# Kernel optimization log

Hardware: AMD Instinct MI355X
Metric: run time of the kernel (lower is better)

The kernel has to match this reference:

```python
import jax, jax.numpy as jnp
import numpy as np

EPS_F = 1e-6   # epsilon_F global in original repo
GAMMA = 0.8
K = 5
BN_EPS = 1e-5
M = 128
N = 100000
E = 1600000
MY = 10

def setup_inputs() -> dict:
    key = jax.random.key(0)
    ks = jax.random.split(key, 6)
    X = jax.random.normal(ks[0], (M, N), dtype=jnp.float32)
    # xavier_uniform for F: limit = sqrt(6/(m+m))
    lim = float(np.sqrt(6.0 / (M + M)))
    F_mat = jax.random.uniform(ks[1], (M, M), dtype=jnp.float32, minval=-lim, maxval=lim)
    B = (1.0 / np.sqrt(M)) * jax.random.normal(ks[2], (MY, M), dtype=jnp.float32)
    bn_weight = jnp.ones((M,), dtype=jnp.float32)
    bn_bias = jnp.zeros((M,), dtype=jnp.float32)
    edge_val = jax.random.uniform(ks[3], (E,), dtype=jnp.float32)
    edge_row = jax.random.randint(ks[4], (E,), 0, N, dtype=jnp.int64 if jax.config.jax_enable_x64 else jnp.int32)
    edge_col = jax.random.randint(ks[5], (E,), 0, N, dtype=jnp.int64 if jax.config.jax_enable_x64 else jnp.int32)
    return {"X": X, "F_mat": F_mat, "B": B, "bn_weight": bn_weight,
            "bn_bias": bn_bias, "edge_val": edge_val,
            "edge_row": edge_row, "edge_col": edge_col}

def reference(X, F_mat, B, bn_weight, bn_bias, edge_val, edge_row, edge_col):
    n = X.shape[1]
    # normalized Gram matrix g(F) = F^T F / (||F^T F||_fro + eps)
    FF = F_mat.T @ F_mat                       # [m, m]
    G = FF / (jnp.linalg.norm(FF) + EPS_F)
    X_first = X                                # [m, n]

    def step(Xc, _):
        Y = Xc.T                               # [n, m]
        # SpMM: (S_t @ Y)[r] += val * Y[c]
        SY = jax.ops.segment_sum(edge_val[:, None] * Y[edge_col], edge_row,
                                 num_segments=n)   # [n, m]
        Xn = GAMMA * (G @ SY.T) + X_first          # [m, n]
        return Xn, None

    Xk, _ = jax.lax.scan(step, X, None, length=K)
    out = Xk.T                                 # [n, m]
    # BatchNorm1d over feature dim (training-mode batch stats); dropout omitted (eval)
    mu = out.mean(axis=0)
    var = out.var(axis=0)
    out = (out - mu) * jax.lax.rsqrt(var + BN_EPS) * bn_weight + bn_bias
    return out @ B.T                           # [n, m_y]
```

## Files before the change

### kernel.cpp

```cpp
#include <hip/hip_runtime.h>
#include <math.h>

#define MDIM 128
#define MY 10
#define GAMMA 0.8f
#define KITER 5
#define CSHIFT 13
#define CCHUNK 13
#define SCAN_BLK 8192

__device__ __forceinline__ float bf2f(unsigned short h) {
    return __uint_as_float(((unsigned int)h) << 16);
}
__device__ __forceinline__ unsigned short f2bf(float f) {
    unsigned int u = __float_as_uint(f);
    u += 0x7fffu + ((u >> 16) & 1u);
    return (unsigned short)(u >> 16);
}

__global__ void k_transpose(const float* __restrict__ X, float* __restrict__ Y0,
                            unsigned short* __restrict__ Y0h, int n) {
    __shared__ float tile[32][33];
    int r0 = blockIdx.x * 32;
    int f0 = blockIdx.y * 32;
    int tx = threadIdx.x, ty = threadIdx.y;
    #pragma unroll
    for (int i = 0; i < 32; i += 8) {
        tile[ty + i][tx] = X[(size_t)(f0 + ty + i) * n + (r0 + tx)];
    }
    __syncthreads();
    #pragma unroll
    for (int i = 0; i < 32; i += 8) {
        float v = tile[tx][ty + i];
        Y0[(size_t)(r0 + ty + i) * MDIM + (f0 + tx)] = v;
        Y0h[(size_t)(r0 + ty + i) * MDIM + (f0 + tx)] = f2bf(v);
    }
}

__global__ void k_gram(const float* __restrict__ F, float* __restrict__ FF,
                       float* __restrict__ normAcc) {
    int i = blockIdx.x, j = threadIdx.x;
    float acc = 0.f;
    for (int k = 0; k < MDIM; ++k)
        acc = fmaf(F[k * MDIM + i], F[k * MDIM + j], acc);
    FF[i * MDIM + j] = acc;
    __shared__ float red[MDIM];
    red[j] = acc * acc;
    __syncthreads();
    for (int s = 64; s > 0; s >>= 1) {
        if (j < s) red[j] += red[j + s];
        __syncthreads();
    }
    if (j == 0) atomicAdd(normAcc, red[0]);
}

__global__ void k_gnorm(const float* __restrict__ FF, const float* __restrict__ normAcc,
                        float* __restrict__ G) {
    int idx = blockIdx.x * 256 + threadIdx.x;
    float s = GAMMA / (sqrtf(*normAcc) + 1e-6f);
    G[idx] = FF[idx] * s;
}

__global__ void k_hist(const int* __restrict__ erow, const int* __restrict__ ecol,
                       int* __restrict__ cnt, int E) {
    int e = blockIdx.x * 256 + threadIdx.x;
    if (e < E) atomicAdd(&cnt[erow[e] * CCHUNK + (ecol[e] >> CSHIFT)], 1);
}

__global__ void k_scan1(const int* __restrict__ cnt, int* __restrict__ blockSums, int nC) {
    int tid = threadIdx.x;
    int base = blockIdx.x * SCAN_BLK + tid * 32;
    int s = 0;
    if (base + 31 < nC) {
        #pragma unroll
        for (int i = 0; i < 8; ++i) {
            int4 v = *(const int4*)&cnt[base + i * 4];
            s += v.x + v.y + v.z + v.w;
        }
    } else {
        for (int i = 0; i < 32; ++i)
            if (base + i < nC) s += cnt[base + i];
    }
    __shared__ int red[256];
    red[tid] = s;
    __syncthreads();
    for (int st = 128; st > 0; st >>= 1) {
        if (tid < st) red[tid] += red[tid + st];
        __syncthreads();
    }
    if (tid == 0) blockSums[blockIdx.x] = red[0];
}

__global__ void k_scan2(int* __restrict__ blockSums, int* __restrict__ rc_off,
                        int nb, int nC) {
    __shared__ int s[256];
    int tid = threadIdx.x;
    int v = (tid < nb) ? blockSums[tid] : 0;
    s[tid] = v;
    __syncthreads();
    for (int off = 1; off < 256; off <<= 1) {
        int t = (tid >= off) ? s[tid - off] : 0;
        __syncthreads();
        s[tid] += t;
        __syncthreads();
    }
    if (tid < nb) blockSums[tid] = s[tid] - v;
    if (tid == 0) rc_off[nC] = s[255];
}

__global__ void k_scan3(const int* __restrict__ cnt, const int* __restrict__ blockOff,
                        int* __restrict__ rc_off, int nC) {
    int tid = threadIdx.x;
    int base = blockIdx.x * SCAN_BLK + tid * 32;
    int v[32];
    #pragma unroll
    for (int i = 0; i < 32; ++i) v[i] = (base + i < nC) ? cnt[base + i] : 0;
    int local = 0;
    #pragma unroll
    for (int i = 0; i < 32; ++i) local += v[i];
    __shared__ int s[256];
    s[tid] = local;
    __syncthreads();
    for (int off = 1; off < 256; off <<= 1) {
        int t = (tid >= off) ? s[tid - off] : 0;
        __syncthreads();
        s[tid] += t;
        __syncthreads();
    }
    int excl = s[tid] - local + blockOff[blockIdx.x];
    #pragma unroll
    for (int i = 0; i < 32; ++i) {
        if (base + i < nC) { rc_off[base + i] = excl; excl += v[i]; }
    }
}

__global__ void k_scatter(const int* __restrict__ erow, const int* __restrict__ ecol,
                          const float* __restrict__ eval_, int* __restrict__ cursor,
                          int2* __restrict__ csr_cv, int E) {
    int e = blockIdx.x * 256 + threadIdx.x;
    if (e < E) {
        int r = erow[e];
        int c = ecol[e];
        int pos = atomicAdd(&cursor[r * CCHUNK + (c >> CSHIFT)], 1);
        csr_cv[pos] = make_int2(c << 8, __float_as_int(eval_[e]));
    }
}

__global__ void __launch_bounds__(256, 8) k_fused(const unsigned short* __restrict__ Yh,
                                                  const int* __restrict__ rc_off,
                                                  const int2* __restrict__ csr_cv,
                                                  const float* __restrict__ G,
                                                  const float* __restrict__ Y0,
                                                  float* __restrict__ Yout,
                                                  unsigned short* __restrict__ Yhout,
                                                  float* __restrict__ stats,
                                                  int writeH, int writeF, int n) {
    __shared__ float sSY[32 * MDIM];
    int tid = threadIdx.x;
    int ty = tid >> 5;
    int tx = tid & 31;
    int rbase = blockIdx.x * 32;
    const char* yb = (const char*)Yh;
    int lbo = tx * 8;

    for (int i = 0; i < 4; ++i) {
        int rloc = ty * 4 + i;
        int e0 = rc_off[(rbase + rloc) * CCHUNK];
        int e1 = rc_off[(rbase + rloc) * CCHUNK + CCHUNK];
        float4 a = make_float4(0.f, 0.f, 0.f, 0.f);
        int e = e0;
        for (; e + 4 <= e1; e += 4) {
            int2 p0 = csr_cv[e + 0];
            int2 p1 = csr_cv[e + 1];
            int2 p2 = csr_cv[e + 2];
            int2 p3 = csr_cv[e + 3];
            ushort4 h0 = *(const ushort4*)(yb + (size_t)(p0.x + lbo));
            ushort4 h1 = *(const ushort4*)(yb + (size_t)(p1.x + lbo));
            ushort4 h2 = *(const ushort4*)(yb + (size_t)(p2.x + lbo));
            ushort4 h3 = *(const ushort4*)(yb + (size_t)(p3.x + lbo));
            float v0 = __int_as_float(p0.y);
            float v1 = __int_as_float(p1.y);
            float v2 = __int_as_float(p2.y);
            float v3 = __int_as_float(p3.y);
            a.x = fmaf(v0, bf2f(h0.x), a.x);
            a.y = fmaf(v0, bf2f(h0.y), a.y);
            a.z = fmaf(v0, bf2f(h0.z), a.z);
            a.w = fmaf(v0, bf2f(h0.w), a.w);
            a.x = fmaf(v1, bf2f(h1.x), a.x);
            a.y = fmaf(v1, bf2f(h1.y), a.y);
            a.z = fmaf(v1, bf2f(h1.z), a.z);
            a.w = fmaf(v1, bf2f(h1.w), a.w);
            a.x = fmaf(v2, bf2f(h2.x), a.x);
            a.y = fmaf(v2, bf2f(h2.y), a.y);
            a.z = fmaf(v2, bf2f(h2.z), a.z);
            a.w = fmaf(v2, bf2f(h2.w), a.w);
            a.x = fmaf(v3, bf2f(h3.x), a.x);
            a.y = fmaf(v3, bf2f(h3.y), a.y);
            a.z = fmaf(v3, bf2f(h3.z), a.z);
            a.w = fmaf(v3, bf2f(h3.w), a.w);
        }
        for (; e < e1; ++e) {
            int2 p = csr_cv[e];
            float v = __int_as_float(p.y);
            ushort4 h = *(const ushort4*)(yb + (size_t)(p.x + lbo));
            a.x = fmaf(v, bf2f(h.x), a.x);
            a.y = fmaf(v, bf2f(h.y), a.y);
            a.z = fmaf(v, bf2f(h.z), a.z);
            a.w = fmaf(v, bf2f(h.w), a.w);
        }
        *(float4*)&sSY[rloc * MDIM + tx * 4] = a;
    }

    size_t r0 = (size_t)rbase + ty * 4;
    int f0 = tx * 4;
    float4 acc[4];
    #pragma unroll
    for (int i = 0; i < 4; ++i) acc[i] = make_float4(0.f, 0.f, 0.f, 0.f);

    for (int j = 0; j < MDIM; j += 4) {
        float4 g0 = *(const float4*)&G[(j + 0) * MDIM + f0];
        float4 g1 = *(const float4*)&G[(j + 1) * MDIM + f0];
        float4 g2 = *(const float4*)&G[(j + 2) * MDIM + f0];
        float4 g3 = *(const float4*)&G[(j + 3) * MDIM + f0];
        #pragma unroll
        for (int i = 0; i < 4; ++i) {
            float4 sr = *(const float4*)&sSY[(ty * 4 + i) * MDIM + j];
            acc[i].x = fmaf(sr.x, g0.x, acc[i].x);
            acc[i].y = fmaf(sr.x, g0.y, acc[i].y);
            acc[i].z = fmaf(sr.x, g0.z, acc[i].z);
            acc[i].w = fmaf(sr.x, g0.w, acc[i].w);
            acc[i].x = fmaf(sr.y, g1.x, acc[i].x);
            acc[i].y = fmaf(sr.y, g1.y, acc[i].y);
            acc[i].z = fmaf(sr.y, g1.z, acc[i].z);
            acc[i].w = fmaf(sr.y, g1.w, acc[i].w);
            acc[i].x = fmaf(sr.z, g2.x, acc[i].x);
            acc[i].y = fmaf(sr.z, g2.y, acc[i].y);
            acc[i].z = fmaf(sr.z, g2.z, acc[i].z);
            acc[i].w = fmaf(sr.z, g2.w, acc[i].w);
            acc[i].x = fmaf(sr.w, g3.x, acc[i].x);
            acc[i].y = fmaf(sr.w, g3.y, acc[i].y);
            acc[i].z = fmaf(sr.w, g3.z, acc[i].z);
            acc[i].w = fmaf(sr.w, g3.w, acc[i].w);
        }
    }

    float4 bs = make_float4(0.f, 0.f, 0.f, 0.f);
    float4 bq = make_float4(0.f, 0.f, 0.f, 0.f);
    #pragma unroll
    for (int i = 0; i < 4; ++i) {
        float4 y0 = *(const float4*)&Y0[(r0 + i) * MDIM + f0];
        float4 o;
        o.x = acc[i].x + y0.x;
        o.y = acc[i].y + y0.y;
        o.z = acc[i].z + y0.z;
        o.w = acc[i].w + y0.w;
        if (writeF) {
            *(float4*)&Yout[(r0 + i) * MDIM + f0] = o;
            bs.x += o.x; bs.y += o.y; bs.z += o.z; bs.w += o.w;
            bq.x = fmaf(o.x, o.x, bq.x);
            bq.y = fmaf(o.y, o.y, bq.y);
            bq.z = fmaf(o.z, o.z, bq.z);
            bq.w = fmaf(o.w, o.w, bq.w);
        }
        if (writeH) {
            ushort4 h;
            h.x = f2bf(o.x);
            h.y = f2bf(o.y);
            h.z = f2bf(o.z);
            h.w = f2bf(o.w);
            *(ushort4*)&Yhout[(r0 + i) * MDIM + f0] = h;
        }
    }

    if (writeF) {
        __syncthreads();
        *(float4*)&sSY[ty * MDIM + f0] = bs;
        *(float4*)&sSY[8 * MDIM + ty * MDIM + f0] = bq;
        __syncthreads();
        if (tid < MDIM) {
            float a = 0.f, b = 0.f;
            #pragma unroll
            for (int t = 0; t < 8; ++t) {
                a += sSY[t * MDIM + tid];
                b += sSY[8 * MDIM + t * MDIM + tid];
            }
            atomicAdd(&stats[tid], a);
            atomicAdd(&stats[MDIM + tid], b);
        }
    }
}

__global__ void k_finalize(const float* __restrict__ stats, const float* __restrict__ B,
                           const float* __restrict__ bnw, const float* __restrict__ bnb,
                           float* __restrict__ Bs, float* __restrict__ cvec, int n) {
    int f = threadIdx.x;
    float inv_n = 1.f / (float)n;
    float mu = stats[f] * inv_n;
    float var = stats[MDIM + f] * inv_n - mu * mu;
    float rs = rsqrtf(var + 1e-5f);
    float sw = rs * bnw[f];
    float cv = bnb[f] - mu * sw;
    __shared__ float red[MDIM];
    for (int o = 0; o < MY; ++o) {
        float b = B[o * MDIM + f];
        Bs[o * MDIM + f] = b * sw;
        red[f] = b * cv;
        __syncthreads();
        for (int s = 64; s > 0; s >>= 1) {
            if (f < s) red[f] += red[f + s];
            __syncthreads();
        }
        if (f == 0) cvec[o] = red[0];
        __syncthreads();
    }
}

__global__ void __launch_bounds__(256) k_project(const float* __restrict__ Y,
                                                 const float* __restrict__ Bs,
                                                 const float* __restrict__ cvec,
                                                 float* __restrict__ out, int n) {
    __shared__ float yt[16 * 129];
    __shared__ float sB[MY * 129];
    __shared__ float sc[MY];
    int tid = threadIdx.x;
    size_t rbase = (size_t)blockIdx.x * 16;
    for (int idx = tid; idx < 16 * MDIM; idx += 256) {
        int r = idx >> 7, f = idx & 127;
        yt[r * 129 + f] = Y[(rbase + r) * MDIM + f];
    }
    for (int idx = tid; idx < MY * MDIM; idx += 256) {
        int o = idx >> 7, f = idx & 127;
        sB[o * 129 + f] = Bs[idx];
    }
    if (tid < MY) sc[tid] = cvec[tid];
    __syncthreads();
    if (tid < 16 * MY) {
        int r = tid / MY, o = tid % MY;
        float acc = sc[o];
        for (int f = 0; f < MDIM; ++f)
            acc = fmaf(yt[r * 129 + f], sB[o * 129 + f], acc);
        out[(rbase + r) * MY + o] = acc;
    }
}

extern "C" void kernel_launch(void* const* d_in, const int* in_sizes, int n_in,
                              void* d_out, int out_size, void* d_ws, size_t ws_size,
                              hipStream_t stream) {
    const float* X    = (const float*)d_in[0];
    const float* F    = (const float*)d_in[1];
    const float* B    = (const float*)d_in[2];
    const float* bnw  = (const float*)d_in[3];
    const float* bnb  = (const float*)d_in[4];
    const float* ev   = (const float*)d_in[5];
    const int*   erow = (const int*)d_in[6];
    const int*   ecol = (const int*)d_in[7];
    float* out = (float*)d_out;
    const int n = in_sizes[0] / MDIM;
    const int E = in_sizes[5];
    const int nC = n * CCHUNK;

    char* w = (char*)d_ws;
    size_t off = 0;
    auto carve = [&](size_t bytes) -> void* {
        void* p = w + off;
        off += (bytes + 255) & ~(size_t)255;
        return p;
    };
    float*          Y0    = (float*)carve((size_t)n * MDIM * 4);
    float*          Ycur  = (float*)carve((size_t)n * MDIM * 4);
    unsigned short* Yh_a  = (unsigned short*)carve((size_t)n * MDIM * 2);
    unsigned short* Yh_b  = (unsigned short*)carve((size_t)n * MDIM * 2);
    float* FF        = (float*)carve(MDIM * MDIM * 4);
    float* G         = (float*)carve(MDIM * MDIM * 4);
    int2*  csr_cv    = (int2*)carve((size_t)E * 8);
    int*   rc_off    = (int*)carve((size_t)(nC + 1) * 4);
    int*   cursor    = (int*)carve((size_t)nC * 4);
    int*   cnt       = (int*)carve((size_t)nC * 4);
    int*   blockSums = (int*)carve(1024 * 4);
    float* normAcc   = (float*)carve(4);
    float* stats     = (float*)carve(2 * MDIM * 4);
    float* Bs        = (float*)carve(MY * MDIM * 4);
    float* cvec      = (float*)carve(MY * 4);
    (void)ws_size;

    hipMemsetAsync(cnt, 0, (size_t)nC * 4, stream);
    hipMemsetAsync(normAcc, 0, 4, stream);
    hipMemsetAsync(stats, 0, 2 * MDIM * 4, stream);

    k_transpose<<<dim3(n / 32, MDIM / 32), dim3(32, 8), 0, stream>>>(X, Y0, Yh_a, n);
    k_gram<<<MDIM, MDIM, 0, stream>>>(F, FF, normAcc);
    k_gnorm<<<MDIM * MDIM / 256, 256, 0, stream>>>(FF, normAcc, G);

    const int nb = (nC + SCAN_BLK - 1) / SCAN_BLK;
    k_hist<<<(E + 255) / 256, 256, 0, stream>>>(erow, ecol, cnt, E);
    k_scan1<<<nb, 256, 0, stream>>>(cnt, blockSums, nC);
    k_scan2<<<1, 256, 0, stream>>>(blockSums, rc_off, nb, nC);
    k_scan3<<<nb, 256, 0, stream>>>(cnt, blockSums, rc_off, nC);
    hipMemcpyAsync(cursor, rc_off, (size_t)nC * 4, hipMemcpyDeviceToDevice, stream);
    k_scatter<<<(E + 255) / 256, 256, 0, stream>>>(erow, ecol, ev, cursor, csr_cv, E);

    for (int k = 0; k < KITER; ++k) {
        const unsigned short* hin = (k & 1) ? Yh_b : Yh_a;
        unsigned short*       hout = (k & 1) ? Yh_a : Yh_b;
        int writeH = (k < KITER - 1) ? 1 : 0;
        int writeF = (k == KITER - 1) ? 1 : 0;
        k_fused<<<n / 32, 256, 0, stream>>>(hin, rc_off, csr_cv, G, Y0, Ycur, hout,
                                            stats, writeH, writeF, n);
    }

    k_finalize<<<1, MDIM, 0, stream>>>(stats, B, bnw, bnb, Bs, cvec, n);
    k_project<<<n / 16, 256, 0, stream>>>(Ycur, Bs, cvec, out, n);
}
```

Before: 934.0 us.

## Reorder CSR chunk-major, process 64 rows per block with interleaved edge streams

The CSR bucketing changes from row-major to column-chunk-major, so each chunk's edges across all rows are grouped and the gathered Y columns stay within an 8K-row window that can remain in cache. Each block now handles two 32-row tiles and walks four rows' edge lists at once, giving more independent gathers in flight. Intermediate iterations read the X_first residual as bf16 instead of fp32 to cut traffic. This costs more rc_off lookups, loop overhead from the chunk loop and per-edge branches, and adds bf16 rounding to the residual in the early iterations.

```diff
diff --git a/kernel.cpp b/kernel.cpp
--- a/kernel.cpp
+++ b/kernel.cpp
@@ -19,7 +19,8 @@
 }
 
 __global__ void k_transpose(const float* __restrict__ X, float* __restrict__ Y0,
-                            unsigned short* __restrict__ Y0h, int n) {
+                            unsigned short* __restrict__ Y0h,
+                            unsigned short* __restrict__ Yh0, int n) {
     __shared__ float tile[32][33];
     int r0 = blockIdx.x * 32;
     int f0 = blockIdx.y * 32;
@@ -32,8 +33,10 @@
     #pragma unroll
     for (int i = 0; i < 32; i += 8) {
         float v = tile[tx][ty + i];
+        unsigned short h = f2bf(v);
         Y0[(size_t)(r0 + ty + i) * MDIM + (f0 + tx)] = v;
-        Y0h[(size_t)(r0 + ty + i) * MDIM + (f0 + tx)] = f2bf(v);
+        Y0h[(size_t)(r0 + ty + i) * MDIM + (f0 + tx)] = h;
+        Yh0[(size_t)(r0 + ty + i) * MDIM + (f0 + tx)] = h;
     }
 }
 
@@ -62,9 +65,9 @@
 }
 
 __global__ void k_hist(const int* __restrict__ erow, const int* __restrict__ ecol,
-                       int* __restrict__ cnt, int E) {
+                       int* __restrict__ cnt, int E, int n) {
     int e = blockIdx.x * 256 + threadIdx.x;
-    if (e < E) atomicAdd(&cnt[erow[e] * CCHUNK + (ecol[e] >> CSHIFT)], 1);
+    if (e < E) atomicAdd(&cnt[(ecol[e] >> CSHIFT) * n + erow[e]], 1);
 }
 
 __global__ void k_scan1(const int* __restrict__ cnt, int* __restrict__ blockSums, int nC) {
@@ -136,21 +139,33 @@
 
 __global__ void k_scatter(const int* __restrict__ erow, const int* __restrict__ ecol,
                           const float* __restrict__ eval_, int* __restrict__ cursor,
-                          int2* __restrict__ csr_cv, int E) {
+                          int2* __restrict__ csr_cv, int E, int n) {
     int e = blockIdx.x * 256 + threadIdx.x;
     if (e < E) {
         int r = erow[e];
         int c = ecol[e];
-        int pos = atomicAdd(&cursor[r * CCHUNK + (c >> CSHIFT)], 1);
+        int pos = atomicAdd(&cursor[(c >> CSHIFT) * n + r], 1);
         csr_cv[pos] = make_int2(c << 8, __float_as_int(eval_[e]));
     }
 }
+
+#define EDGE_STEP(eCur, eEnd, acc)                                        \
+    if (eCur < eEnd) {                                                    \
+        int2 p = csr_cv[eCur++];                                          \
+        float v = __int_as_float(p.y);                                    \
+        ushort4 h = *(const ushort4*)(yb + (size_t)(p.x + lbo));          \
+        acc.x = fmaf(v, bf2f(h.x), acc.x);                                \
+        acc.y = fmaf(v, bf2f(h.y), acc.y);                                \
+        acc.z = fmaf(v, bf2f(h.z), acc.z);                                \
+        acc.w = fmaf(v, bf2f(h.w), acc.w);                                \
+    }
 
 __global__ void __launch_bounds__(256, 8) k_fused(const unsigned short* __restrict__ Yh,
                                                   const int* __restrict__ rc_off,
                                                   const int2* __restrict__ csr_cv,
                                                   const float* __restrict__ G,
                                                   const float* __restrict__ Y0,
+                                                  const unsigned short* __restrict__ Y0h,
                                                   float* __restrict__ Yout,
                                                   unsigned short* __restrict__ Yhout,
                                                   float* __restrict__ stats,
@@ -159,116 +174,118 @@
     int tid = threadIdx.x;
     int ty = tid >> 5;
     int tx = tid & 31;
-    int rbase = blockIdx.x * 32;
+    int rbase0 = blockIdx.x * 64;
+    int rbase1 = rbase0 + 32;
+    bool hasT1 = (rbase1 < n);
     const char* yb = (const char*)Yh;
     int lbo = tx * 8;
 
-    for (int i = 0; i < 4; ++i) {
-        int rloc = ty * 4 + i;
-        int e0 = rc_off[(rbase + rloc) * CCHUNK];
-        int e1 = rc_off[(rbase + rloc) * CCHUNK + CCHUNK];
-        float4 a = make_float4(0.f, 0.f, 0.f, 0.f);
-        int e = e0;
-        for (; e + 4 <= e1; e += 4) {
-            int2 p0 = csr_cv[e + 0];
-            int2 p1 = csr_cv[e + 1];
-            int2 p2 = csr_cv[e + 2];
-            int2 p3 = csr_cv[e + 3];
-            ushort4 h0 = *(const ushort4*)(yb + (size_t)(p0.x + lbo));
-            ushort4 h1 = *(const ushort4*)(yb + (size_t)(p1.x + lbo));
-            ushort4 h2 = *(const ushort4*)(yb + (size_t)(p2.x + lbo));
-            ushort4 h3 = *(const ushort4*)(yb + (size_t)(p3.x + lbo));
-            float v0 = __int_as_float(p0.y);
-            float v1 = __int_as_float(p1.y);
-            float v2 = __int_as_float(p2.y);
-            float v3 = __int_as_float(p3.y);
-            a.x = fmaf(v0, bf2f(h0.x), a.x);
-            a.y = fmaf(v0, bf2f(h0.y), a.y);
-            a.z = fmaf(v0, bf2f(h0.z), a.z);
-            a.w = fmaf(v0, bf2f(h0.w), a.w);
-            a.x = fmaf(v1, bf2f(h1.x), a.x);
-            a.y = fmaf(v1, bf2f(h1.y), a.y);
-            a.z = fmaf(v1, bf2f(h1.z), a.z);
-            a.w = fmaf(v1, bf2f(h1.w), a.w);
-            a.x = fmaf(v2, bf2f(h2.x), a.x);
-            a.y = fmaf(v2, bf2f(h2.y), a.y);
-            a.z = fmaf(v2, bf2f(h2.z), a.z);
-            a.w = fmaf(v2, bf2f(h2.w), a.w);
-            a.x = fmaf(v3, bf2f(h3.x), a.x);
-            a.y = fmaf(v3, bf2f(h3.y), a.y);
-            a.z = fmaf(v3, bf2f(h3.z), a.z);
-            a.w = fmaf(v3, bf2f(h3.w), a.w);
-        }
-        for (; e < e1; ++e) {
-            int2 p = csr_cv[e];
-            float v = __int_as_float(p.y);
-            ushort4 h = *(const ushort4*)(yb + (size_t)(p.x + lbo));
-            a.x = fmaf(v, bf2f(h.x), a.x);
-            a.y = fmaf(v, bf2f(h.y), a.y);
-            a.z = fmaf(v, bf2f(h.z), a.z);
-            a.w = fmaf(v, bf2f(h.w), a.w);
-        }
-        *(float4*)&sSY[rloc * MDIM + tx * 4] = a;
-    }
-
-    size_t r0 = (size_t)rbase + ty * 4;
+    float4 a0 = make_float4(0.f, 0.f, 0.f, 0.f);
+    float4 a1 = a0, a2 = a0, a3 = a0;
+    float4 b0 = a0, b1 = a0, b2 = a0, b3 = a0;
+
+    for (int c = 0; c < CCHUNK; ++c) {
+        {
+            int base = c * n + rbase0 + ty * 4;
+            int4 bb = *(const int4*)&rc_off[base];
+            int b4 = rc_off[base + 4];
+            int e0 = bb.x, e1 = bb.y, e2 = bb.z, e3 = bb.w;
+            while ((e0 < bb.y) | (e1 < bb.z) | (e2 < bb.w) | (e3 < b4)) {
+                EDGE_STEP(e0, bb.y, a0)
+                EDGE_STEP(e1, bb.z, a1)
+                EDGE_STEP(e2, bb.w, a2)
+                EDGE_STEP(e3, b4, a3)
+            }
+        }
+        if (hasT1) {
+            int base = c * n + rbase1 + ty * 4;
+            int4 bb = *(const int4*)&rc_off[base];
+            int b4 = rc_off[base + 4];
+            int e0 = bb.x, e1 = bb.y, e2 = bb.z, e3 = bb.w;
+            while ((e0 < bb.y) | (e1 < bb.z) | (e2 < bb.w) | (e3 < b4)) {
+                EDGE_STEP(e0, bb.y, b0)
+                EDGE_STEP(e1, bb.z, b1)
+                EDGE_STEP(e2, bb.w, b2)
+                EDGE_STEP(e3, b4, b3)
+            }
+        }
+    }
+
     int f0 = tx * 4;
-    float4 acc[4];
-    #pragma unroll
-    for (int i = 0; i < 4; ++i) acc[i] = make_float4(0.f, 0.f, 0.f, 0.f);
-
-    for (int j = 0; j < MDIM; j += 4) {
-        float4 g0 = *(const float4*)&G[(j + 0) * MDIM + f0];
-        float4 g1 = *(const float4*)&G[(j + 1) * MDIM + f0];
-        float4 g2 = *(const float4*)&G[(j + 2) * MDIM + f0];
-        float4 g3 = *(const float4*)&G[(j + 3) * MDIM + f0];
+    float4 bs = make_float4(0.f, 0.f, 0.f, 0.f);
+    float4 bq = make_float4(0.f, 0.f, 0.f, 0.f);
+
+    for (int t = 0; t < 2; ++t) {
+        if (t == 1 && !hasT1) break;
+        *(float4*)&sSY[(ty * 4 + 0) * MDIM + f0] = (t == 0) ? a0 : b0;
+        *(float4*)&sSY[(ty * 4 + 1) * MDIM + f0] = (t == 0) ? a1 : b1;
+        *(float4*)&sSY[(ty * 4 + 2) * MDIM + f0] = (t == 0) ? a2 : b2;
+        *(float4*)&sSY[(ty * 4 + 3) * MDIM + f0] = (t == 0) ? a3 : b3;
+
+        size_t r0 = (size_t)(t == 0 ? rbase0 : rbase1) + ty * 4;
+        float4 acc[4];
+        #pragma unroll
+        for (int i = 0; i < 4; ++i) acc[i] = make_float4(0.f, 0.f, 0.f, 0.f);
+        for (int j = 0; j < MDIM; j += 4) {
+            float4 g0 = *(const float4*)&G[(j + 0) * MDIM + f0];
+            float4 g1 = *(const float4*)&G[(j + 1) * MDIM + f0];
+            float4 g2 = *(const float4*)&G[(j + 2) * MDIM + f0];
+            float4 g3 = *(const float4*)&G[(j + 3) * MDIM + f0];
+            #pragma unroll
+            for (int i = 0; i < 4; ++i) {
+                float4 sr = *(const float4*)&sSY[(ty * 4 + i) * MDIM + j];
+                acc[i].x = fmaf(sr.x, g0.x, acc[i].x);
+                acc[i].y = fmaf(sr.x, g0.y, acc[i].y);
+                acc[i].z = fmaf(sr.x, g0.z, acc[i].z);
+                acc[i].w = fmaf(sr.x, g0.w, acc[i].w);
+                acc[i].x = fmaf(sr.y, g1.x, acc[i].x);
+                acc[i].y = fmaf(sr.y, g1.y, acc[i].y);
+                acc[i].z = fmaf(sr.y, g1.z, acc[i].z);
+                acc[i].w = fmaf(sr.y, g1.w, acc[i].w);
+                acc[i].x = fmaf(sr.z, g2.x, acc[i].x);
+                acc[i].y = fmaf(sr.z, g2.y, acc[i].y);
+                acc[i].z = fmaf(sr.z, g2.z, acc[i].z);
+                acc[i].w = fmaf(sr.z, g2.w, acc[i].w);
+                acc[i].x = fmaf(sr.w, g3.x, acc[i].x);
+                acc[i].y = fmaf(sr.w, g3.y, acc[i].y);
+                acc[i].z = fmaf(sr.w, g3.z, acc[i].z);
+                acc[i].w = fmaf(sr.w, g3.w, acc[i].w);
+            }
+        }
+
         #pragma unroll
         for (int i = 0; i < 4; ++i) {
-            float4 sr = *(const float4*)&sSY[(ty * 4 + i) * MDIM + j];
-            acc[i].x = fmaf(sr.x, g0.x, acc[i].x);
-            acc[i].y = fmaf(sr.x, g0.y, acc[i].y);
-            acc[i].z = fmaf(sr.x, g0.z, acc[i].z);
-            acc[i].w = fmaf(sr.x, g0.w, acc[i].w);
-            acc[i].x = fmaf(sr.y, g1.x, acc[i].x);
-            acc[i].y = fmaf(sr.y, g1.y, acc[i].y);
-            acc[i].z = fmaf(sr.y, g1.z, acc[i].z);
-            acc[i].w = fmaf(sr.y, g1.w, acc[i].w);
-            acc[i].x = fmaf(sr.z, g2.x, acc[i].x);
-            acc[i].y = fmaf(sr.z, g2.y, acc[i].y);
-            acc[i].z = fmaf(sr.z, g2.z, acc[i].z);
-            acc[i].w = fmaf(sr.z, g2.w, acc[i].w);
-            acc[i].x = fmaf(sr.w, g3.x, acc[i].x);
-            acc[i].y = fmaf(sr.w, g3.y, acc[i].y);
-            acc[i].z = fmaf(sr.w, g3.z, acc[i].z);
-            acc[i].w = fmaf(sr.w, g3.w, acc[i].w);
-        }
-    }
-
-    float4 bs = make_float4(0.f, 0.f, 0.f, 0.f);
-    float4 bq = make_float4(0.f, 0.f, 0.f, 0.f);
-    #pragma unroll
-    for (int i = 0; i < 4; ++i) {
-        float4 y0 = *(const float4*)&Y0[(r0 + i) * MDIM + f0];
-        float4 o;
-        o.x = acc[i].x + y0.x;
-        o.y = acc[i].y + y0.y;
-        o.z = acc[i].z + y0.z;
-        o.w = acc[i].w + y0.w;
-        if (writeF) {
-            *(float4*)&Yout[(r0 + i) * MDIM + f0] = o;
-            bs.x += o.x; bs.y += o.y; bs.z += o.z; bs.w += o.w;
-            bq.x = fmaf(o.x, o.x, bq.x);
-            bq.y = fmaf(o.y, o.y, bq.y);
-            bq.z = fmaf(o.z, o.z, bq.z);
-            bq.w = fmaf(o.w, o.w, bq.w);
-        }
-        if (writeH) {
-            ushort4 h;
-            h.x = f2bf(o.x);
-            h.y = f2bf(o.y);
-            h.z = f2bf(o.z);
-            h.w = f2bf(o.w);
-            *(ushort4*)&Yhout[(r0 + i) * MDIM + f0] = h;
+            float4 y0;
+            if (writeF) {
+                y0 = *(const float4*)&Y0[(r0 + i) * MDIM + f0];
+            } else {
+                ushort4 t4 = *(const ushort4*)&Y0h[(r0 + i) * MDIM + f0];
+                y0.x = bf2f(t4.x);
+                y0.y = bf2f(t4.y);
+                y0.z = bf2f(t4.z);
+                y0.w = bf2f(t4.w);
+            }
+            float4 o;
+            o.x = acc[i].x + y0.x;
+            o.y = acc[i].y + y0.y;
+            o.z = acc[i].z + y0.z;
+            o.w = acc[i].w + y0.w;
+            if (writeF) {
+                *(float4*)&Yout[(r0 + i) * MDIM + f0] = o;
+                bs.x += o.x; bs.y += o.y; bs.z += o.z; bs.w += o.w;
+                bq.x = fmaf(o.x, o.x, bq.x);
+                bq.y = fmaf(o.y, o.y, bq.y);
+                bq.z = fmaf(o.z, o.z, bq.z);
+                bq.w = fmaf(o.w, o.w, bq.w);
+            }
+            if (writeH) {
+                ushort4 h;
+                h.x = f2bf(o.x);
+                h.y = f2bf(o.y);
+                h.z = f2bf(o.z);
+                h.w = f2bf(o.w);
+                *(ushort4*)&Yhout[(r0 + i) * MDIM + f0] = h;
+            }
         }
     }
 
@@ -368,6 +385,7 @@
     };
     float*          Y0    = (float*)carve((size_t)n * MDIM * 4);
     float*          Ycur  = (float*)carve((size_t)n * MDIM * 4);
+    unsigned short* Y0h   = (unsigned short*)carve((size_t)n * MDIM * 2);
     unsigned short* Yh_a  = (unsigned short*)carve((size_t)n * MDIM * 2);
     unsigned short* Yh_b  = (unsigned short*)carve((size_t)n * MDIM * 2);
     float* FF        = (float*)carve(MDIM * MDIM * 4);
@@ -387,25 +405,26 @@
     hipMemsetAsync(normAcc, 0, 4, stream);
     hipMemsetAsync(stats, 0, 2 * MDIM * 4, stream);
 
-    k_transpose<<<dim3(n / 32, MDIM / 32), dim3(32, 8), 0, stream>>>(X, Y0, Yh_a, n);
+    k_transpose<<<dim3(n / 32, MDIM / 32), dim3(32, 8), 0, stream>>>(X, Y0, Y0h, Yh_a, n);
     k_gram<<<MDIM, MDIM, 0, stream>>>(F, FF, normAcc);
     k_gnorm<<<MDIM * MDIM / 256, 256, 0, stream>>>(FF, normAcc, G);
 
     const int nb = (nC + SCAN_BLK - 1) / SCAN_BLK;
-    k_hist<<<(E + 255) / 256, 256, 0, stream>>>(erow, ecol, cnt, E);
+    k_hist<<<(E + 255) / 256, 256, 0, stream>>>(erow, ecol, cnt, E, n);
     k_scan1<<<nb, 256, 0, stream>>>(cnt, blockSums, nC);
     k_scan2<<<1, 256, 0, stream>>>(blockSums, rc_off, nb, nC);
     k_scan3<<<nb, 256, 0, stream>>>(cnt, blockSums, rc_off, nC);
     hipMemcpyAsync(cursor, rc_off, (size_t)nC * 4, hipMemcpyDeviceToDevice, stream);
-    k_scatter<<<(E + 255) / 256, 256, 0, stream>>>(erow, ecol, ev, cursor, csr_cv, E);
-
+    k_scatter<<<(E + 255) / 256, 256, 0, stream>>>(erow, ecol, ev, cursor, csr_cv, E, n);
+
+    const int nblk = (n + 63) / 64;
     for (int k = 0; k < KITER; ++k) {
         const unsigned short* hin = (k & 1) ? Yh_b : Yh_a;
         unsigned short*       hout = (k & 1) ? Yh_a : Yh_b;
         int writeH = (k < KITER - 1) ? 1 : 0;
         int writeF = (k == KITER - 1) ? 1 : 0;
-        k_fused<<<n / 32, 256, 0, stream>>>(hin, rc_off, csr_cv, G, Y0, Ycur, hout,
-                                            stats, writeH, writeF, n);
+        k_fused<<<nblk, 256, 0, stream>>>(hin, rc_off, csr_cv, G, Y0, Y0h, Ycur, hout,
+                                          stats, writeH, writeF, n);
     }
 
     k_finalize<<<1, MDIM, 0, stream>>>(stats, B, bnw, bnb, Bs, cvec, n);
```

After: 1.514 ms. +62.1%, slower.
